# Kernel tuning notes

Hardware: AMD Instinct MI355X
Metric: run time of the kernel (lower is better)

The kernel has to match this reference:

```python
import jax, jax.numpy as jnp
import numpy as np

EMBD_DIM = 1024
HEAD_SIZE = 64


def setup_inputs() -> dict:
    key = jax.random.key(0)
    kx, kq, kk, kv = jax.random.split(key, 4)
    x = jax.random.normal(kx, (4, 4096, EMBD_DIM), dtype=jnp.float32)
    # nn.Linear(embd_dim, head_size, bias=False) weights, stored as [C, H] so x @ W
    s = 1.0 / np.sqrt(EMBD_DIM)
    Wq = jax.random.uniform(kq, (EMBD_DIM, HEAD_SIZE), jnp.float32, -s, s)
    Wk = jax.random.uniform(kk, (EMBD_DIM, HEAD_SIZE), jnp.float32, -s, s)
    Wv = jax.random.uniform(kv, (EMBD_DIM, HEAD_SIZE), jnp.float32, -s, s)
    return {"x": x, "Wq": Wq, "Wk": Wk, "Wv": Wv}


def reference(x, Wq, Wk, Wv):
    # q,k,v: [B, T, H]
    q = jnp.einsum("btc,ch->bth", x, Wq)
    k = jnp.einsum("btc,ch->bth", x, Wk)
    v = jnp.einsum("btc,ch->bth", x, Wv)
    scale = k.shape[-1] ** -0.5
    # full [B, T, T] score matrix, as in the original naive implementation
    scores = jnp.einsum("bth,bsh->bts", q, k) * scale
    attn = jax.nn.softmax(scores, axis=-1)
    # dropout p=0.0 -> identity
    out = jnp.einsum("bts,bsh->bth", attn, v)  # [B, T, H]
    return out
```

## Files before the change

### kernel.cpp

```cpp
#include <hip/hip_runtime.h>
#include <hip/hip_bf16.h>

#define B_ 4
#define T_ 4096
#define C_ 1024
#define H_ 64

typedef float  f32x4  __attribute__((ext_vector_type(4)));
typedef short  bf16x8 __attribute__((ext_vector_type(8)));
typedef uint   u32x4  __attribute__((ext_vector_type(4)));

static __device__ __forceinline__ ushort f2bf(float f) {
  union { float f; uint u; } v; v.f = f;
  uint u = v.u;
  u += 0x7FFFu + ((u >> 16) & 1u);
  return (ushort)(u >> 16);
}

static __device__ __forceinline__ uint cvtpk(float s0, float s1) {
  uint r;
  asm("v_cvt_pk_bf16_f32 %0, %1, %2" : "=v"(r) : "v"(s0), "v"(s1));
  return r;
}

static __device__ __forceinline__ void gload_lds16(const void* g, void* l) {
  __builtin_amdgcn_global_load_lds(
      (const __attribute__((address_space(1))) unsigned int*)g,
      (__attribute__((address_space(3))) unsigned int*)l, 16, 0, 0);
}

#define MFMA(a, b, c) __builtin_amdgcn_mfma_f32_16x16x32_bf16(a, b, c, 0, 0, 0)

__global__ __launch_bounds__(256) void wt_prep(const float* __restrict__ Wq,
                                               const float* __restrict__ Wk,
                                               const float* __restrict__ Wv,
                                               ushort* __restrict__ WtF) {
  int idx = blockIdx.x * 256 + threadIdx.x;
  int j = idx & 7, lane = (idx >> 3) & 63, nt = (idx >> 9) & 3;
  int kc = (idx >> 11) & 1, c64 = (idx >> 12) & 15, w = idx >> 16;
  int l15 = lane & 15, g = lane >> 4;
  int c = c64 * 64 + kc * 32 + g * 8 + j;
  int n = nt * 16 + l15;
  const float* W = (w == 0) ? Wq : (w == 1) ? Wk : Wv;
  WtF[idx] = f2bf(W[c * 64 + n]);
}

__global__ __launch_bounds__(256) void qkv_proj(const float* __restrict__ x,
                                                const ushort* __restrict__ WtF,
                                                ushort* __restrict__ Qg,
                                                char* __restrict__ Kb,
                                                char* __restrict__ VaF) {
  __shared__ __align__(16) ushort wl[2][12288];
  const int tid = threadIdx.x;
  const int lane = tid & 63, wid = tid >> 6;
  const int l15 = lane & 15, g = lane >> 4;
  const int b = blockIdx.x >> 6, rt = blockIdx.x & 63;
  const int wrow = rt * 64 + wid * 16;

  f32x4 acc[3][4];
  #pragma unroll
  for (int w = 0; w < 3; w++)
    #pragma unroll
    for (int nt = 0; nt < 4; nt++) acc[w][nt] = (f32x4)0.0f;

  const float* xr = x + ((size_t)b * T_ + wrow + l15) * C_ + g * 8;

  auto stagew = [&](int buf, int c64) {
    char* dst = (char*)wl[buf] + tid * 16;
    const char* src = (const char*)WtF + (size_t)c64 * 8192 + tid * 16;
    #pragma unroll
    for (int p = 0; p < 6; p++)
      gload_lds16(src + (p >> 1) * 131072 + (p & 1) * 4096, dst + p * 4096);
  };

  f32x4 xp[2][4];
  stagew(0, 0);
  #pragma unroll
  for (int i = 0; i < 2; i++) {
    xp[0][2 * i]     = *(const f32x4*)(xr + i * 32);
    xp[0][2 * i + 1] = *(const f32x4*)(xr + i * 32 + 4);
  }
  __syncthreads();

  #pragma unroll
  for (int t = 0; t < 16; t++) {
    const int cur = t & 1;
    if (t < 15) {
      stagew(cur ^ 1, t + 1);
      const float* nx = xr + (t + 1) * 64;
      #pragma unroll
      for (int i = 0; i < 2; i++) {
        xp[cur ^ 1][2 * i]     = *(const f32x4*)(nx + i * 32);
        xp[cur ^ 1][2 * i + 1] = *(const f32x4*)(nx + i * 32 + 4);
      }
    }
    bf16x8 xa[2];
    #pragma unroll
    for (int kc = 0; kc < 2; kc++) {
      union { uint u[4]; bf16x8 v; } h;
      f32x4 c0 = xp[cur][2 * kc], c1 = xp[cur][2 * kc + 1];
      h.u[0] = cvtpk(c0[0], c0[1]); h.u[1] = cvtpk(c0[2], c0[3]);
      h.u[2] = cvtpk(c1[0], c1[1]); h.u[3] = cvtpk(c1[2], c1[3]);
      xa[kc] = h.v;
    }
    const char* wb = (const char*)wl[cur] + lane * 16;
    __builtin_amdgcn_s_setprio(1);
    #pragma unroll
    for (int w = 0; w < 3; w++)
      #pragma unroll
      for (int kc = 0; kc < 2; kc++)
        #pragma unroll
        for (int nt = 0; nt < 4; nt++) {
          bf16x8 wf = *(const bf16x8*)(wb + w * 8192 + kc * 4096 + nt * 1024);
          acc[w][nt] = MFMA(xa[kc], wf, acc[w][nt]);
        }
    __builtin_amdgcn_s_setprio(0);
    __syncthreads();
  }

  char* kdst = Kb + ((size_t)b * 64 + rt) * 8192;
  char* vdst = VaF + ((size_t)b * 128 + (wrow >> 5)) * 4096;
  #pragma unroll
  for (int nt = 0; nt < 4; nt++) {
    int n = nt * 16 + l15;
    #pragma unroll
    for (int r = 0; r < 4; r++) {
      int tt = wrow + g * 4 + r;
      Qg[((size_t)b * T_ + tt) * H_ + n] = f2bf(acc[0][nt][r]);
      int key = tt & 63;
      *(ushort*)(kdst + ((key * 128 + n * 2) ^ ((key & 7) << 4))) = f2bf(acc[1][nt][r]);
      int k5 = tt & 31;
      int gp = ((k5 >> 4) << 1) | ((k5 >> 2) & 1);
      int js = ((k5 >> 3) & 1) * 4 + (k5 & 3);
      *(ushort*)(vdst + nt * 1024 + (gp * 16 + l15) * 16 + js * 2) = f2bf(acc[2][nt][r]);
    }
  }
}

__global__ __launch_bounds__(256) void attn(const ushort* __restrict__ Qg,
                                            const char* __restrict__ Kb,
                                            const char* __restrict__ VaF,
                                            float* __restrict__ Op,
                                            float* __restrict__ Ds,
                                            float* __restrict__ out,
                                            int KT) {
  __shared__ __align__(16) char kv[2][16384];
  const int tid = threadIdx.x;
  const int lane = tid & 63, wid = tid >> 6;
  const int bid = blockIdx.x;
  const int s = bid >> 7, r7 = bid & 127;
  const int b = r7 >> 5, qt = r7 & 31;
  const int l15 = lane & 15, g = lane >> 4;

  bf16x8 qa[2][2];
  #pragma unroll
  for (int qs = 0; qs < 2; qs++) {
    const ushort* qp = Qg + ((size_t)b * T_ + qt * 128 + wid * 32 + qs * 16 + l15) * H_ + g * 8;
    qa[qs][0] = *(const bf16x8*)qp;
    qa[qs][1] = *(const bf16x8*)(qp + 32);
  }

  f32x4 oacc[2][4];
  #pragma unroll
  for (int qs = 0; qs < 2; qs++)
    #pragma unroll
    for (int nt = 0; nt < 4; nt++) oacc[qs][nt] = (f32x4)0.0f;
  float dsum[2] = {0.f, 0.f};

  const char* kbase = Kb + (size_t)b * 64 * 8192;
  const char* vbase = VaF + (size_t)b * 128 * 4096;
  const int it0 = s * KT;

  auto stage = [&](int buf, int it) {
    char* dst = kv[buf] + tid * 16;
    const char* ks = kbase + (size_t)it * 8192 + tid * 16;
    const char* vs = vbase + (size_t)it * 8192 + tid * 16;
    gload_lds16(ks, dst);
    gload_lds16(ks + 4096, dst + 4096);
    gload_lds16(vs, dst + 8192);
    gload_lds16(vs + 4096, dst + 12288);
  };

  stage(0, it0);
  __syncthreads();

  for (int it = 0; it < KT; it++) {
    const int cur = it & 1;
    if (it + 1 < KT) stage(cur ^ 1, it0 + it + 1);
    const char* kl = kv[cur];
    const char* vl = kv[cur] + 8192;

    f32x4 sacc[2][4];
    #pragma unroll
    for (int qs = 0; qs < 2; qs++)
      #pragma unroll
      for (int nt = 0; nt < 4; nt++) sacc[qs][nt] = (f32x4)0.0f;
    __builtin_amdgcn_s_setprio(1);
    #pragma unroll
    for (int nt = 0; nt < 4; nt++) {
      int kr = nt * 16 + l15;
      bf16x8 ka0 = *(const bf16x8*)(kl + ((kr * 128 + g * 16) ^ ((kr & 7) << 4)));
      bf16x8 ka1 = *(const bf16x8*)(kl + ((kr * 128 + 64 + g * 16) ^ ((kr & 7) << 4)));
      #pragma unroll
      for (int qs = 0; qs < 2; qs++) {
        sacc[qs][nt] = MFMA(ka0, qa[qs][0], sacc[qs][nt]);
        sacc[qs][nt] = MFMA(ka1, qa[qs][1], sacc[qs][nt]);
      }
    }
    __builtin_amdgcn_s_setprio(0);

    uint t0[2][4], t1[2][4];
    #pragma unroll
    for (int qs = 0; qs < 2; qs++)
      #pragma unroll
      for (int nt = 0; nt < 4; nt++) {
        float p0 = __builtin_amdgcn_exp2f(sacc[qs][nt][0] * 0.18033688011112042f);
        float p1 = __builtin_amdgcn_exp2f(sacc[qs][nt][1] * 0.18033688011112042f);
        float p2 = __builtin_amdgcn_exp2f(sacc[qs][nt][2] * 0.18033688011112042f);
        float p3 = __builtin_amdgcn_exp2f(sacc[qs][nt][3] * 0.18033688011112042f);
        dsum[qs] += (p0 + p1) + (p2 + p3);
        t0[qs][nt] = cvtpk(p0, p1);
        t1[qs][nt] = cvtpk(p2, p3);
      }

    #pragma unroll
    for (int kk = 0; kk < 2; kk++) {
      bf16x8 pf[2];
      #pragma unroll
      for (int qs = 0; qs < 2; qs++) {
        uint x0 = t0[qs][2 * kk], y0 = t0[qs][2 * kk + 1];
        uint x1 = t1[qs][2 * kk], y1 = t1[qs][2 * kk + 1];
        asm volatile("v_permlane32_swap_b32 %0, %1" : "+v"(x0), "+v"(y0));
        asm volatile("v_permlane32_swap_b32 %0, %1" : "+v"(x1), "+v"(y1));
        union { uint u[4]; bf16x8 v; } pfu;
        pfu.u[0] = x0; pfu.u[1] = x1; pfu.u[2] = y0; pfu.u[3] = y1;
        pf[qs] = pfu.v;
      }
      __builtin_amdgcn_s_setprio(1);
      #pragma unroll
      for (int ntd = 0; ntd < 4; ntd++) {
        bf16x8 va = *(const bf16x8*)(vl + kk * 4096 + ntd * 1024 + lane * 16);
        oacc[0][ntd] = MFMA(va, pf[0], oacc[0][ntd]);
        oacc[1][ntd] = MFMA(va, pf[1], oacc[1][ntd]);
      }
      __builtin_amdgcn_s_setprio(0);
    }
    __syncthreads();
  }

  #pragma unroll
  for (int qs = 0; qs < 2; qs++) {
    float d = dsum[qs];
    d += __shfl_xor(d, 16, 64);
    d += __shfl_xor(d, 32, 64);
    const int q = qt * 128 + wid * 32 + qs * 16 + l15;
    if (Op != nullptr) {
      float* ob = Op + ((size_t)(s * 4 + b) * T_ + q) * H_;
      #pragma unroll
      for (int nt = 0; nt < 4; nt++)
        #pragma unroll
        for (int r = 0; r < 4; r++) ob[nt * 16 + g * 4 + r] = oacc[qs][nt][r];
      if (g == 0) Ds[(size_t)(s * 4 + b) * T_ + q] = d;
    } else {
      float inv = 1.0f / d;
      float* ob = out + ((size_t)b * T_ + q) * H_;
      #pragma unroll
      for (int nt = 0; nt < 4; nt++)
        #pragma unroll
        for (int r = 0; r < 4; r++) ob[nt * 16 + g * 4 + r] = oacc[qs][nt][r] * inv;
    }
  }
}

__global__ __launch_bounds__(256) void reduce_seg(const float* __restrict__ Op,
                                                  const float* __restrict__ Ds,
                                                  float* __restrict__ out, int seg) {
  int i = blockIdx.x * 256 + threadIdx.x;
  size_t e = (size_t)i * 4;
  int row = (int)(e >> 6);
  f32x4 o = (f32x4)0.0f;
  float d = 0.0f;
  for (int s = 0; s < seg; s++) {
    o += *(const f32x4*)(Op + (size_t)s * (4u * T_ * H_) + e);
    d += Ds[(size_t)s * (4u * T_) + row];
  }
  *(f32x4*)(out + e) = o * (1.0f / d);
}

extern "C" void kernel_launch(void* const* d_in, const int* in_sizes, int n_in,
                              void* d_out, int out_size, void* d_ws, size_t ws_size,
                              hipStream_t stream) {
  const float* x  = (const float*)d_in[0];
  const float* Wq = (const float*)d_in[1];
  const float* Wk = (const float*)d_in[2];
  const float* Wv = (const float*)d_in[3];
  float* out = (float*)d_out;

  char* ws = (char*)d_ws;
  size_t off = 0;
  auto take = [&](size_t n) -> void* {
    void* p = ws + off;
    off = (off + n + 255) & ~(size_t)255;
    return p;
  };
  ushort* Qg  = (ushort*)take((size_t)B_ * T_ * H_ * 2);
  char*   Kb  = (char*)take((size_t)B_ * T_ * H_ * 2);
  char*   VaF = (char*)take((size_t)B_ * T_ * H_ * 2);
  ushort* WtF = (ushort*)take((size_t)3 * H_ * C_ * 2);

  int seg = 1;
  float* Op = nullptr;
  float* Ds = nullptr;
  for (int sg = 4; sg >= 2; sg >>= 1) {
    size_t need = off + (size_t)sg * B_ * T_ * H_ * 4 + 256 + (size_t)sg * B_ * T_ * 4 + 256;
    if (need <= ws_size) {
      seg = sg;
      Op = (float*)take((size_t)sg * B_ * T_ * H_ * 4);
      Ds = (float*)take((size_t)sg * B_ * T_ * 4);
      break;
    }
  }
  int KT = 64 / seg;

  wt_prep<<<768, 256, 0, stream>>>(Wq, Wk, Wv, WtF);
  qkv_proj<<<B_ * 64, 256, 0, stream>>>(x, WtF, Qg, Kb, VaF);
  attn<<<B_ * (T_ / 128) * seg, 256, 0, stream>>>(Qg, Kb, VaF, Op, Ds, out, KT);
  if (Op) reduce_seg<<<(B_ * T_ * H_ / 4 + 255) / 256, 256, 0, stream>>>(Op, Ds, out, seg);
}
```

Before: 61.63 us.

## Load K/V fragments directly to registers in attention, drop LDS staging

The attention kernel no longer stages K/V tiles through LDS with block barriers. Each wave now loads K and V fragments straight from global memory into registers, in a new MFMA-fragment K layout written by the projection kernel, and prefetches K for the next tile using ping-pong register sets. The block index mapping is reordered so batch varies fastest, and launch bounds request two blocks per CU. The projection kernel gains a three-deep x prefetch with explicit vmcnt waits in place of __syncthreads. The aim is to remove LDS round-trips and barrier stalls, at the cost of every wave redundantly fetching K/V through cache and higher register pressure.

```diff
diff --git a/kernel.cpp b/kernel.cpp
--- a/kernel.cpp
+++ b/kernel.cpp
@@ -48,7 +48,7 @@
 __global__ __launch_bounds__(256) void qkv_proj(const float* __restrict__ x,
                                                 const ushort* __restrict__ WtF,
                                                 ushort* __restrict__ Qg,
-                                                char* __restrict__ Kb,
+                                                char* __restrict__ KaF,
                                                 char* __restrict__ VaF) {
   __shared__ __align__(16) ushort wl[2][12288];
   const int tid = threadIdx.x;
@@ -73,32 +73,34 @@
       gload_lds16(src + (p >> 1) * 131072 + (p & 1) * 4096, dst + p * 4096);
   };
 
-  f32x4 xp[2][4];
+  f32x4 xp[3][4];
+  auto xload = [&](int slot, int t) {
+    const float* src = xr + t * 64;
+    xp[slot][0] = *(const f32x4*)src;
+    xp[slot][1] = *(const f32x4*)(src + 4);
+    xp[slot][2] = *(const f32x4*)(src + 32);
+    xp[slot][3] = *(const f32x4*)(src + 36);
+  };
+
   stagew(0, 0);
-  #pragma unroll
-  for (int i = 0; i < 2; i++) {
-    xp[0][2 * i]     = *(const f32x4*)(xr + i * 32);
-    xp[0][2 * i + 1] = *(const f32x4*)(xr + i * 32 + 4);
-  }
-  __syncthreads();
+  xload(0, 0);
+  xload(1, 1);
+  asm volatile("s_waitcnt vmcnt(8)" ::: "memory");
+  __builtin_amdgcn_s_barrier();
+  __builtin_amdgcn_sched_barrier(0);
 
   #pragma unroll
   for (int t = 0; t < 16; t++) {
     const int cur = t & 1;
-    if (t < 15) {
-      stagew(cur ^ 1, t + 1);
-      const float* nx = xr + (t + 1) * 64;
-      #pragma unroll
-      for (int i = 0; i < 2; i++) {
-        xp[cur ^ 1][2 * i]     = *(const f32x4*)(nx + i * 32);
-        xp[cur ^ 1][2 * i + 1] = *(const f32x4*)(nx + i * 32 + 4);
-      }
-    }
+    if (t < 15) stagew(cur ^ 1, t + 1);
+    if (t < 14) xload((t + 2) % 3, t + 2);
+
+    const int slot = t % 3;
     bf16x8 xa[2];
     #pragma unroll
     for (int kc = 0; kc < 2; kc++) {
       union { uint u[4]; bf16x8 v; } h;
-      f32x4 c0 = xp[cur][2 * kc], c1 = xp[cur][2 * kc + 1];
+      f32x4 c0 = xp[slot][2 * kc], c1 = xp[slot][2 * kc + 1];
       h.u[0] = cvtpk(c0[0], c0[1]); h.u[1] = cvtpk(c0[2], c0[3]);
       h.u[2] = cvtpk(c1[0], c1[1]); h.u[3] = cvtpk(c1[2], c1[3]);
       xa[kc] = h.v;
@@ -115,20 +117,28 @@
           acc[w][nt] = MFMA(xa[kc], wf, acc[w][nt]);
         }
     __builtin_amdgcn_s_setprio(0);
-    __syncthreads();
-  }
-
-  char* kdst = Kb + ((size_t)b * 64 + rt) * 8192;
+
+    if (t < 15) {
+      if (t < 14) asm volatile("s_waitcnt vmcnt(4)" ::: "memory");
+      else        asm volatile("s_waitcnt vmcnt(0)" ::: "memory");
+      __builtin_amdgcn_s_barrier();
+      __builtin_amdgcn_sched_barrier(0);
+    }
+  }
+
+  char* kdst = KaF + ((size_t)b * 64 + rt) * 8192;
   char* vdst = VaF + ((size_t)b * 128 + (wrow >> 5)) * 4096;
   #pragma unroll
   for (int nt = 0; nt < 4; nt++) {
     int n = nt * 16 + l15;
+    int kc = n >> 5, gp2 = (n >> 3) & 3, j2 = n & 7;
     #pragma unroll
     for (int r = 0; r < 4; r++) {
       int tt = wrow + g * 4 + r;
       Qg[((size_t)b * T_ + tt) * H_ + n] = f2bf(acc[0][nt][r]);
       int key = tt & 63;
-      *(ushort*)(kdst + ((key * 128 + n * 2) ^ ((key & 7) << 4))) = f2bf(acc[1][nt][r]);
+      *(ushort*)(kdst + kc * 4096 + (key >> 4) * 1024 +
+                 (gp2 * 16 + (key & 15)) * 16 + j2 * 2) = f2bf(acc[1][nt][r]);
       int k5 = tt & 31;
       int gp = ((k5 >> 4) << 1) | ((k5 >> 2) & 1);
       int js = ((k5 >> 3) & 1) * 4 + (k5 & 3);
@@ -137,19 +147,19 @@
   }
 }
 
-__global__ __launch_bounds__(256) void attn(const ushort* __restrict__ Qg,
-                                            const char* __restrict__ Kb,
-                                            const char* __restrict__ VaF,
-                                            float* __restrict__ Op,
-                                            float* __restrict__ Ds,
-                                            float* __restrict__ out,
-                                            int KT) {
-  __shared__ __align__(16) char kv[2][16384];
+__global__ __launch_bounds__(256, 2) void attn(const ushort* __restrict__ Qg,
+                                               const char* __restrict__ KaF,
+                                               const char* __restrict__ VaF,
+                                               float* __restrict__ Op,
+                                               float* __restrict__ Ds,
+                                               float* __restrict__ out,
+                                               int KT) {
   const int tid = threadIdx.x;
   const int lane = tid & 63, wid = tid >> 6;
   const int bid = blockIdx.x;
-  const int s = bid >> 7, r7 = bid & 127;
-  const int b = r7 >> 5, qt = r7 & 31;
+  const int b = bid & 3;
+  const int r2 = bid >> 2;
+  const int qt = r2 & 31, s = r2 >> 5;
   const int l15 = lane & 15, g = lane >> 4;
 
   bf16x8 qa[2][2];
@@ -167,28 +177,22 @@
     for (int nt = 0; nt < 4; nt++) oacc[qs][nt] = (f32x4)0.0f;
   float dsum[2] = {0.f, 0.f};
 
-  const char* kbase = Kb + (size_t)b * 64 * 8192;
+  const char* kbase = KaF + (size_t)b * 64 * 8192;
   const char* vbase = VaF + (size_t)b * 128 * 4096;
   const int it0 = s * KT;
 
-  auto stage = [&](int buf, int it) {
-    char* dst = kv[buf] + tid * 16;
-    const char* ks = kbase + (size_t)it * 8192 + tid * 16;
-    const char* vs = vbase + (size_t)it * 8192 + tid * 16;
-    gload_lds16(ks, dst);
-    gload_lds16(ks + 4096, dst + 4096);
-    gload_lds16(vs, dst + 8192);
-    gload_lds16(vs + 4096, dst + 12288);
-  };
-
-  stage(0, it0);
-  __syncthreads();
-
-  for (int it = 0; it < KT; it++) {
-    const int cur = it & 1;
-    if (it + 1 < KT) stage(cur ^ 1, it0 + it + 1);
-    const char* kl = kv[cur];
-    const char* vl = kv[cur] + 8192;
+  bf16x8 kaA[8], kaB[8];
+  {
+    const char* kt = kbase + (size_t)it0 * 8192 + lane * 16;
+    #pragma unroll
+    for (int i = 0; i < 8; i++) kaA[i] = *(const bf16x8*)(kt + i * 1024);
+  }
+
+  auto body = [&](int it, bf16x8 (&kaC)[8], bf16x8 (&kaN)[8]) {
+    const char* vt = vbase + (size_t)(it0 + it) * 8192 + lane * 16;
+    bf16x8 va[8];
+    #pragma unroll
+    for (int i = 0; i < 8; i++) va[i] = *(const bf16x8*)(vt + i * 1024);
 
     f32x4 sacc[2][4];
     #pragma unroll
@@ -197,17 +201,19 @@
       for (int nt = 0; nt < 4; nt++) sacc[qs][nt] = (f32x4)0.0f;
     __builtin_amdgcn_s_setprio(1);
     #pragma unroll
-    for (int nt = 0; nt < 4; nt++) {
-      int kr = nt * 16 + l15;
-      bf16x8 ka0 = *(const bf16x8*)(kl + ((kr * 128 + g * 16) ^ ((kr & 7) << 4)));
-      bf16x8 ka1 = *(const bf16x8*)(kl + ((kr * 128 + 64 + g * 16) ^ ((kr & 7) << 4)));
+    for (int nt = 0; nt < 4; nt++)
       #pragma unroll
       for (int qs = 0; qs < 2; qs++) {
-        sacc[qs][nt] = MFMA(ka0, qa[qs][0], sacc[qs][nt]);
-        sacc[qs][nt] = MFMA(ka1, qa[qs][1], sacc[qs][nt]);
+        sacc[qs][nt] = MFMA(kaC[nt], qa[qs][0], sacc[qs][nt]);
+        sacc[qs][nt] = MFMA(kaC[4 + nt], qa[qs][1], sacc[qs][nt]);
       }
-    }
     __builtin_amdgcn_s_setprio(0);
+
+    if (it + 1 < KT) {
+      const char* kt = kbase + (size_t)(it0 + it + 1) * 8192 + lane * 16;
+      #pragma unroll
+      for (int i = 0; i < 8; i++) kaN[i] = *(const bf16x8*)(kt + i * 1024);
+    }
 
     uint t0[2][4], t1[2][4];
     #pragma unroll
@@ -239,13 +245,16 @@
       __builtin_amdgcn_s_setprio(1);
       #pragma unroll
       for (int ntd = 0; ntd < 4; ntd++) {
-        bf16x8 va = *(const bf16x8*)(vl + kk * 4096 + ntd * 1024 + lane * 16);
-        oacc[0][ntd] = MFMA(va, pf[0], oacc[0][ntd]);
-        oacc[1][ntd] = MFMA(va, pf[1], oacc[1][ntd]);
+        oacc[0][ntd] = MFMA(va[kk * 4 + ntd], pf[0], oacc[0][ntd]);
+        oacc[1][ntd] = MFMA(va[kk * 4 + ntd], pf[1], oacc[1][ntd]);
       }
       __builtin_amdgcn_s_setprio(0);
     }
-    __syncthreads();
+  };
+
+  for (int it = 0; it < KT; it += 2) {
+    body(it, kaA, kaB);
+    body(it + 1, kaB, kaA);
   }
 
   #pragma unroll
@@ -304,7 +313,7 @@
     return p;
   };
   ushort* Qg  = (ushort*)take((size_t)B_ * T_ * H_ * 2);
-  char*   Kb  = (char*)take((size_t)B_ * T_ * H_ * 2);
+  char*   KaF = (char*)take((size_t)B_ * T_ * H_ * 2);
   char*   VaF = (char*)take((size_t)B_ * T_ * H_ * 2);
   ushort* WtF = (ushort*)take((size_t)3 * H_ * C_ * 2);
 
@@ -323,7 +332,7 @@
   int KT = 64 / seg;
 
   wt_prep<<<768, 256, 0, stream>>>(Wq, Wk, Wv, WtF);
-  qkv_proj<<<B_ * 64, 256, 0, stream>>>(x, WtF, Qg, Kb, VaF);
-  attn<<<B_ * (T_ / 128) * seg, 256, 0, stream>>>(Qg, Kb, VaF, Op, Ds, out, KT);
+  qkv_proj<<<B_ * 64, 256, 0, stream>>>(x, WtF, Qg, KaF, VaF);
+  attn<<<B_ * (T_ / 128) * seg, 256, 0, stream>>>(Qg, KaF, VaF, Op, Ds, out, KT);
   if (Op) reduce_seg<<<(B_ * T_ * H_ / 4 + 255) / 256, 256, 0, stream>>>(Op, Ds, out, seg);
 }
```

Result: faster. 54.88 us (-11.0%).
